# Optimization experiments

Hardware: AMD Instinct MI355X
Metric: run time of the kernel (lower is better)

The kernel has to match this reference:

```python
import jax, jax.numpy as jnp
import numpy as np

# gen_dx_bx([-30,30,0.15], [-15,15,0.15])
DX = jnp.array([0.15, 0.15], dtype=jnp.float32)
BX = jnp.array([-29.925, -14.925], dtype=jnp.float32)


def _pairwise_dist(a, b):
    # torch.cdist p=2: [Na,2] x [Nb,2] -> [Na,Nb]
    return jnp.sqrt(jnp.sum((a[:, None, :] - b[None, :, :]) ** 2, axis=-1))


def _single(match, position, semantic, pts, ins, typ):
    # match [M,M] (M=N+1 with dustbin), position [N,2], semantic [C,N],
    # pts [G,2], ins [G] int, typ [G] int. Assumes mask is all-ones (set in setup_inputs).
    N = position.shape[0]
    M = match.shape[0]
    G = pts.shape[0]
    C = semantic.shape[0]

    pos = position * DX + BX                      # grid -> meters
    cd = _pairwise_dist(pos, pts)                 # [N,G]
    nearest = cd.argmin(-1).astype(jnp.int32)     # [N]
    cdist_mean = jnp.mean(cd.min(-1))             # mean of per-pred nearest-GT distance
    dist_map = _pairwise_dist(pos, pos)           # [N,N]
    nmax = nearest.max()

    # precompute, for every gt index g, whether any pred maps to it and the
    # closest such pred (torch: idx_pred_next[cdist[idx_pred_next, g].argmin()])
    assign = nearest[:, None] == jnp.arange(G, dtype=jnp.int32)[None, :]  # [N,G]
    exists_g = assign.any(0)                                              # [G]
    best_pred_g = jnp.where(assign, cd, jnp.inf).argmin(0).astype(jnp.int32)  # [G]

    def walk(start_gt):
        # greedy forward walk along gt indices; replicates the python while-loop,
        # including torch's negative-index wrap (idx % G) for idx_gt_next = -1.
        def cond(st):
            return ~st[2]

        def body(st):
            idx, steps, done, res = st
            is_end = idx >= nmax
            g_next_raw = jnp.where(is_end, jnp.int32(-1), idx + 1)
            g_next = jnp.mod(g_next_raw, G)
            ex = (~is_end) & exists_g[g_next]  # nearest==-1 never holds in torch
            same = ins[jnp.mod(idx, G)] == ins[g_next]
            matched = ex & same
            stop = matched | (~same) | (steps >= G + 2)  # safety bound
            res_new = jnp.where(matched, best_pred_g[g_next], jnp.int32(-1))
            return (g_next_raw, steps + jnp.int32(1), stop, res_new)

        st = (start_gt, jnp.int32(0), jnp.bool_(False), jnp.int32(-1))
        return jax.lax.while_loop(cond, body, st)[3]

    next_pred = jax.vmap(walk)(nearest)  # [N], -1 means no match (dustbin later)

    # build match_gt [M,M]
    A = jnp.zeros((M, M), dtype=match.dtype)
    valid = next_pred >= 0
    cols = jnp.where(valid, next_pred, 0)
    A = A.at[jnp.arange(N), cols].max(valid.astype(match.dtype))

    # resolve columns matched by multiple rows: keep the row closest in dist_map
    Acols = A[:, :N]
    col_sum = Acols.sum(0)
    dist_pad = jnp.concatenate([dist_map, jnp.full((1, N), jnp.inf, dist_map.dtype)], 0)  # [M,N]
    keep = jnp.where(Acols > 0, dist_pad, jnp.inf).argmin(0)  # [N]
    onehot = (jnp.arange(M)[:, None] == keep[None, :]).astype(match.dtype)
    Acols = jnp.where(col_sum[None, :] > 1, onehot, Acols)
    A = A.at[:, :N].set(Acols)

    # unmatched pred rows -> dustbin column; unmatched pred cols -> dustbin row
    row_sum = A[:N].sum(1)
    A = A.at[:N, M - 1].set(jnp.where(row_sum == 0, 1.0, A[:N, M - 1]))
    col_sum2 = A[:, :N].sum(0)
    A = A.at[M - 1, :N].set(jnp.where(col_sum2 == 0, 1.0, A[M - 1, :N]))

    # semantic gt: one-hot of the type of each pred's nearest gt point
    cls = typ[nearest]  # [N]
    semantic_gt = (jnp.arange(C)[:, None] == cls[None, :]).astype(semantic.dtype)  # [C,N]

    # NLL match loss (torch transposes then feeds NLLLoss: loss = -match[j, target[j]])
    tgt_b = A.argmax(0)  # per-column gt row
    tgt_f = A.argmax(1)  # per-row gt col
    j = jnp.arange(M - 1)
    loss_b = -jnp.mean(match[j, tgt_b[: M - 1]])
    loss_f = -jnp.mean(match[j, tgt_f[: M - 1]])
    match_loss = 0.5 * (loss_f + loss_b)

    sem_loss = -jnp.mean(semantic[semantic_gt.argmax(0), jnp.arange(N)])
    return cdist_mean, match_loss, sem_loss, A, semantic_gt


def setup_inputs() -> dict:
    key = jax.random.key(0)
    ks = jax.random.split(key, 5)
    B, N, G, C, NI = 4, 2048, 1024, 3, 32
    # log-probability score matrix with dustbin (Sinkhorn-style output)
    matches = jax.nn.log_softmax(jax.random.normal(ks[0], (B, N + 1, N + 1), jnp.float32), axis=-1)
    # predicted vertex grid coords on the 400x200 BEV grid
    positions = jax.random.uniform(ks[1], (B, N, 2), jnp.float32) * jnp.array([400.0, 200.0], jnp.float32)
    semantics = jax.nn.log_softmax(jax.random.normal(ks[2], (B, C, N), jnp.float32), axis=1)
    masks = jnp.ones((B, N, 1), jnp.float32)
    # gt points in meters within the BEV range
    gt_pts = (jax.random.uniform(ks[3], (B, G, 2), jnp.float32) - 0.5) * jnp.array([60.0, 30.0], jnp.float32)
    # sorted instance ids -> contiguous runs like the original per-instance list build
    gt_ins = jnp.sort(jax.random.randint(ks[4], (B, G), 0, NI), axis=-1).astype(jnp.int32)
    gt_type = (gt_ins % C).astype(jnp.int32)
    return {"matches": matches, "positions": positions, "semantics": semantics,
            "masks": masks, "gt_pts": gt_pts, "gt_ins": gt_ins, "gt_type": gt_type}


def reference(matches, positions, semantics, masks, gt_pts, gt_ins, gt_type):
    cm, ml, sl, mg, sg = jax.vmap(_single)(matches, positions, semantics, gt_pts, gt_ins, gt_type)
    # reduction='mean'
    return jnp.mean(cm), jnp.mean(ml), jnp.mean(sl), mg, sg
```

## Files before the change

### kernel.cpp

```cpp
#include <hip/hip_runtime.h>
#include <math.h>

#define BB 4
#define NN 2048
#define GG 1024
#define CC 3
#define MM 2049

typedef unsigned long long u64;
#define KEY_EMPTY 0xFFFFFFFFFFFFFFFFULL

struct Ws {
  int   nearest[BB * NN];
  u64   best_key[BB * GG];
  u64   keep_key[BB * NN];
  int   next_pred[BB * NN];
  int   col_cnt[BB * NN];
  int   nmax[BB];
  float cdist_sum[BB];
  float sem_sum[BB];
  float lossf_sum[BB];
  float lossb_sum[BB];
};

__device__ __forceinline__ float posx(float p) { return __fadd_rn(__fmul_rn(p, 0.15f), -29.925f); }
__device__ __forceinline__ float posy(float p) { return __fadd_rn(__fmul_rn(p, 0.15f), -14.925f); }
__device__ __forceinline__ float pdist(float ax, float ay, float bx, float by) {
  float dx = __fsub_rn(ax, bx);
  float dy = __fsub_rn(ay, by);
  return __fsqrt_rn(__fadd_rn(__fmul_rn(dx, dx), __fmul_rn(dy, dy)));
}
__device__ __forceinline__ u64 pack_key(float d, int i) {
  return ((u64)__float_as_uint(d) << 32) | (unsigned int)i;
}


__global__ void k_zero(float* __restrict__ out, int n) {
  int n4 = n >> 2;
  float4 z = make_float4(0.f, 0.f, 0.f, 0.f);
  for (int t = blockIdx.x * blockDim.x + threadIdx.x; t < n4; t += gridDim.x * blockDim.x)
    reinterpret_cast<float4*>(out)[t] = z;
  int t = blockIdx.x * blockDim.x + threadIdx.x;
  int tail = n & 3;
  if (t < tail) out[n4 * 4 + t] = 0.f;
}

__global__ void k_init(Ws* ws) {
  int t = blockIdx.x * blockDim.x + threadIdx.x;
  if (t < BB * NN) {
    ws->col_cnt[t] = 0;
    ws->keep_key[t] = KEY_EMPTY;
  }
  if (t < BB * GG) ws->best_key[t] = KEY_EMPTY;
  if (t < BB) {
    ws->nmax[t] = 0;
    ws->cdist_sum[t] = 0.f;
    ws->sem_sum[t] = 0.f;
    ws->lossf_sum[t] = 0.f;
    ws->lossb_sum[t] = 0.f;
  }
}

__global__ __launch_bounds__(256) void k_nearest(const float* __restrict__ positions,
                                                 const float* __restrict__ gt_pts,
                                                 const int* __restrict__ gt_type,
                                                 const float* __restrict__ semantics,
                                                 Ws* ws, float* __restrict__ out) {
  __shared__ float spts[GG * 2];
  __shared__ float sred[4];
  __shared__ int   sredi[4];
  const int bpb = NN / 256;
  int b = blockIdx.x / bpb;
  int i = (blockIdx.x % bpb) * 256 + threadIdx.x;

  for (int t = threadIdx.x; t < GG * 2; t += 256) spts[t] = gt_pts[b * GG * 2 + t];
  __syncthreads();

  float px = posx(positions[(size_t)(b * NN + i) * 2 + 0]);
  float py = posy(positions[(size_t)(b * NN + i) * 2 + 1]);

  float dmin = INFINITY;
  int gmin = 0;
  #pragma unroll 4
  for (int g = 0; g < GG; ++g) {
    float d = pdist(px, py, spts[2 * g], spts[2 * g + 1]);
    if (d < dmin) { dmin = d; gmin = g; }
  }
  ws->nearest[b * NN + i] = gmin;
  atomicMin(&ws->best_key[b * GG + gmin], pack_key(dmin, i));

  int cls = gt_type[b * GG + gmin];
  float* sg = out + 3 + (size_t)BB * MM * MM;
  sg[(size_t)b * CC * NN + 0 * NN + i] = (cls == 0) ? 1.f : 0.f;
  sg[(size_t)b * CC * NN + 1 * NN + i] = (cls == 1) ? 1.f : 0.f;
  sg[(size_t)b * CC * NN + 2 * NN + i] = (cls == 2) ? 1.f : 0.f;
  float sem = semantics[(size_t)b * CC * NN + (size_t)cls * NN + i];

  int lane = threadIdx.x & 63, w = threadIdx.x >> 6;

  float v = dmin;
  #pragma unroll
  for (int o = 32; o > 0; o >>= 1) v += __shfl_down(v, o, 64);
  if (lane == 0) sred[w] = v;
  __syncthreads();
  if (threadIdx.x == 0) atomicAdd(&ws->cdist_sum[b], sred[0] + sred[1] + sred[2] + sred[3]);
  __syncthreads();

  v = sem;
  #pragma unroll
  for (int o = 32; o > 0; o >>= 1) v += __shfl_down(v, o, 64);
  if (lane == 0) sred[w] = v;
  __syncthreads();
  if (threadIdx.x == 0) atomicAdd(&ws->sem_sum[b], sred[0] + sred[1] + sred[2] + sred[3]);
  __syncthreads();

  int m = gmin;
  #pragma unroll
  for (int o = 32; o > 0; o >>= 1) m = max(m, __shfl_down(m, o, 64));
  if (lane == 0) sredi[w] = m;
  __syncthreads();
  if (threadIdx.x == 0)
    atomicMax(&ws->nmax[b], max(max(sredi[0], sredi[1]), max(sredi[2], sredi[3])));
}

__global__ __launch_bounds__(256) void k_walk(const int* __restrict__ gt_ins,
                                              const float* __restrict__ positions, Ws* ws) {
  __shared__ int sins[GG];
  __shared__ int sbest[GG];
  const int bpb = NN / 256;
  int b = blockIdx.x / bpb;
  int i = (blockIdx.x % bpb) * 256 + threadIdx.x;

  for (int t = threadIdx.x; t < GG; t += 256) {
    sins[t] = gt_ins[b * GG + t];
    u64 k = ws->best_key[b * GG + t];
    sbest[t] = (k == KEY_EMPTY) ? -1 : (int)(k & 0xFFFFFFFFULL);
  }
  __syncthreads();

  int nmax = ws->nmax[b];
  int idx = ws->nearest[b * NN + i];
  int steps = 0, res = -1;
  while (true) {
    bool is_end = idx >= nmax;
    int gnr = is_end ? -1 : idx + 1;
    int gn = gnr & (GG - 1);
    bool ex = (!is_end) && (sbest[gn] >= 0);
    bool same = sins[idx & (GG - 1)] == sins[gn];
    bool matched = ex && same;
    res = matched ? sbest[gn] : -1;
    bool stop = matched || (!same) || (steps >= GG + 2);
    idx = gnr;
    ++steps;
    if (stop) break;
  }
  ws->next_pred[b * NN + i] = res;
  if (res >= 0) {
    atomicAdd(&ws->col_cnt[b * NN + res], 1);
    const float* pb = positions + (size_t)b * NN * 2;
    float d = pdist(posx(pb[2 * i]), posy(pb[2 * i + 1]),
                    posx(pb[2 * res]), posy(pb[2 * res + 1]));
    atomicMin(&ws->keep_key[b * NN + res], pack_key(d, i));
  }
}

__global__ __launch_bounds__(256) void k_scatter(Ws* ws, float* __restrict__ out) {
  const int bpb = NN / 256;
  int b = blockIdx.x / bpb;
  int i = (blockIdx.x % bpb) * 256 + threadIdx.x;

  float* A = out + 3 + (size_t)b * MM * MM;

  int j = ws->next_pred[b * NN + i];
  bool surv = (j >= 0) && ((int)(ws->keep_key[b * NN + j] & 0xFFFFFFFFULL) == i);
  if (surv) A[(size_t)i * MM + j] = 1.0f;
  else      A[(size_t)i * MM + (MM - 1)] = 1.0f;

  if (ws->col_cnt[b * NN + i] == 0)
    A[(size_t)(MM - 1) * MM + i] = 1.0f;
}

__global__ __launch_bounds__(256) void k_loss(const float* __restrict__ matches, Ws* ws) {
  __shared__ float sred[4];
  const int bpb = NN / 256;
  int b = blockIdx.x / bpb;
  int k = (blockIdx.x % bpb) * 256 + threadIdx.x;

  int j = ws->next_pred[b * NN + k];
  bool surv = (j >= 0) && ((int)(ws->keep_key[b * NN + j] & 0xFFFFFFFFULL) == k);
  int tf = surv ? j : (MM - 1);
  float vf = matches[(size_t)b * MM * MM + (size_t)k * MM + tf];

  int cnt = ws->col_cnt[b * NN + k];
  int tb = (cnt > 0) ? (int)(ws->keep_key[b * NN + k] & 0xFFFFFFFFULL) : (MM - 1);
  float vb = matches[(size_t)b * MM * MM + (size_t)k * MM + tb];

  int lane = threadIdx.x & 63, w = threadIdx.x >> 6;

  float v = vf;
  #pragma unroll
  for (int o = 32; o > 0; o >>= 1) v += __shfl_down(v, o, 64);
  if (lane == 0) sred[w] = v;
  __syncthreads();
  if (threadIdx.x == 0) atomicAdd(&ws->lossf_sum[b], sred[0] + sred[1] + sred[2] + sred[3]);
  __syncthreads();

  v = vb;
  #pragma unroll
  for (int o = 32; o > 0; o >>= 1) v += __shfl_down(v, o, 64);
  if (lane == 0) sred[w] = v;
  __syncthreads();
  if (threadIdx.x == 0) atomicAdd(&ws->lossb_sum[b], sred[0] + sred[1] + sred[2] + sred[3]);
}

__global__ void k_final(Ws* ws, float* __restrict__ out) {
  if (threadIdx.x == 0 && blockIdx.x == 0) {
    float cm = 0.f, ml = 0.f, sl = 0.f;
    for (int b = 0; b < BB; ++b) {
      cm += ws->cdist_sum[b] / (float)NN;
      float lf = -(ws->lossf_sum[b] / (float)(MM - 1));
      float lb = -(ws->lossb_sum[b] / (float)(MM - 1));
      ml += 0.5f * (lf + lb);
      sl += -(ws->sem_sum[b] / (float)NN);
    }
    out[0] = cm / (float)BB;
    out[1] = ml / (float)BB;
    out[2] = sl / (float)BB;
  }
}

extern "C" void kernel_launch(void* const* d_in, const int* in_sizes, int n_in,
                              void* d_out, int out_size, void* d_ws, size_t ws_size,
                              hipStream_t stream) {
  (void)in_sizes; (void)n_in; (void)ws_size;
  const float* matches   = (const float*)d_in[0];
  const float* positions = (const float*)d_in[1];
  const float* semantics = (const float*)d_in[2];
  const float* gt_pts    = (const float*)d_in[4];
  const int*   gt_ins    = (const int*)d_in[5];
  const int*   gt_type   = (const int*)d_in[6];
  float* out = (float*)d_out;
  Ws* ws = (Ws*)d_ws;

  k_zero<<<2048, 256, 0, stream>>>(out, out_size);
  k_init<<<(BB * NN + 255) / 256, 256, 0, stream>>>(ws);
  k_nearest<<<BB * (NN / 256), 256, 0, stream>>>(positions, gt_pts, gt_type, semantics, ws, out);
  k_walk<<<BB * (NN / 256), 256, 0, stream>>>(gt_ins, positions, ws);
  k_scatter<<<BB * (NN / 256), 256, 0, stream>>>(ws, out);
  k_loss<<<BB * (NN / 256), 256, 0, stream>>>(matches, ws);
  k_final<<<1, 64, 0, stream>>>(ws, out);
}
```

Before: 171.6 us.

## Split nearest-GT search across blocks, fuse scatter/loss, use memset and smaller blocks

The nearest-GT search is split into 8 chunks of GT points per pred. Each chunk is handled by its own block and combined through a packed atomicMin key, so the launch goes from 32 blocks to 256. The per-pred bookkeeping moves to a separate 64-thread kernel. The scatter and loss kernels are merged, the custom zero kernel is replaced with hipMemsetAsync, and the walk and post kernels use 64-thread blocks to spread across more CUs. The split adds an extra kernel launch and more atomics, and ties are still broken by the lowest index because the key packs distance with the index.

```diff
diff --git a/kernel.cpp b/kernel.cpp
--- a/kernel.cpp
+++ b/kernel.cpp
@@ -6,14 +6,17 @@
 #define GG 1024
 #define CC 3
 #define MM 2049
+#define SP 8
+#define CH (GG / SP)
 
 typedef unsigned long long u64;
 #define KEY_EMPTY 0xFFFFFFFFFFFFFFFFULL
 
 struct Ws {
-  int   nearest[BB * NN];
+  u64   near_key[BB * NN];
   u64   best_key[BB * GG];
   u64   keep_key[BB * NN];
+  int   nearest[BB * NN];
   int   next_pred[BB * NN];
   int   col_cnt[BB * NN];
   int   nmax[BB];
@@ -35,21 +38,12 @@
 }
 
 
-__global__ void k_zero(float* __restrict__ out, int n) {
-  int n4 = n >> 2;
-  float4 z = make_float4(0.f, 0.f, 0.f, 0.f);
-  for (int t = blockIdx.x * blockDim.x + threadIdx.x; t < n4; t += gridDim.x * blockDim.x)
-    reinterpret_cast<float4*>(out)[t] = z;
-  int t = blockIdx.x * blockDim.x + threadIdx.x;
-  int tail = n & 3;
-  if (t < tail) out[n4 * 4 + t] = 0.f;
-}
-
 __global__ void k_init(Ws* ws) {
   int t = blockIdx.x * blockDim.x + threadIdx.x;
   if (t < BB * NN) {
+    ws->near_key[t] = KEY_EMPTY;
+    ws->keep_key[t] = KEY_EMPTY;
     ws->col_cnt[t] = 0;
-    ws->keep_key[t] = KEY_EMPTY;
   }
   if (t < BB * GG) ws->best_key[t] = KEY_EMPTY;
   if (t < BB) {
@@ -61,19 +55,16 @@
   }
 }
 
-__global__ __launch_bounds__(256) void k_nearest(const float* __restrict__ positions,
-                                                 const float* __restrict__ gt_pts,
-                                                 const int* __restrict__ gt_type,
-                                                 const float* __restrict__ semantics,
-                                                 Ws* ws, float* __restrict__ out) {
-  __shared__ float spts[GG * 2];
-  __shared__ float sred[4];
-  __shared__ int   sredi[4];
-  const int bpb = NN / 256;
-  int b = blockIdx.x / bpb;
-  int i = (blockIdx.x % bpb) * 256 + threadIdx.x;
-
-  for (int t = threadIdx.x; t < GG * 2; t += 256) spts[t] = gt_pts[b * GG * 2 + t];
+__global__ __launch_bounds__(256) void k_near1(const float* __restrict__ positions,
+                                               const float* __restrict__ gt_pts, Ws* ws) {
+  __shared__ float spts[CH * 2];
+  const int cpb = NN / 256;
+  int b = blockIdx.x / (cpb * SP);
+  int r = blockIdx.x % (cpb * SP);
+  int i = (r / SP) * 256 + threadIdx.x;
+  int g0 = (r % SP) * CH;
+
+  spts[threadIdx.x] = gt_pts[b * GG * 2 + g0 * 2 + threadIdx.x];
   __syncthreads();
 
   float px = posx(positions[(size_t)(b * NN + i) * 2 + 0]);
@@ -82,59 +73,65 @@
   float dmin = INFINITY;
   int gmin = 0;
   #pragma unroll 4
-  for (int g = 0; g < GG; ++g) {
+  for (int g = 0; g < CH; ++g) {
     float d = pdist(px, py, spts[2 * g], spts[2 * g + 1]);
     if (d < dmin) { dmin = d; gmin = g; }
   }
-  ws->nearest[b * NN + i] = gmin;
-  atomicMin(&ws->best_key[b * GG + gmin], pack_key(dmin, i));
-
-  int cls = gt_type[b * GG + gmin];
+  atomicMin(&ws->near_key[b * NN + i], pack_key(dmin, g0 + gmin));
+}
+
+__global__ __launch_bounds__(64) void k_near2(const int* __restrict__ gt_type,
+                                              const float* __restrict__ semantics,
+                                              Ws* ws, float* __restrict__ out) {
+  int b = blockIdx.x >> 5;
+  int i = (blockIdx.x & 31) * 64 + threadIdx.x;
+
+  u64 key = ws->near_key[b * NN + i];
+  float dmin = __uint_as_float((unsigned int)(key >> 32));
+  int g = (int)(key & 0xFFFFFFFFULL);
+
+  ws->nearest[b * NN + i] = g;
+  atomicMin(&ws->best_key[b * GG + g], pack_key(dmin, i));
+
+  int cls = gt_type[b * GG + g];
   float* sg = out + 3 + (size_t)BB * MM * MM;
   sg[(size_t)b * CC * NN + 0 * NN + i] = (cls == 0) ? 1.f : 0.f;
   sg[(size_t)b * CC * NN + 1 * NN + i] = (cls == 1) ? 1.f : 0.f;
   sg[(size_t)b * CC * NN + 2 * NN + i] = (cls == 2) ? 1.f : 0.f;
   float sem = semantics[(size_t)b * CC * NN + (size_t)cls * NN + i];
 
-  int lane = threadIdx.x & 63, w = threadIdx.x >> 6;
-
   float v = dmin;
   #pragma unroll
   for (int o = 32; o > 0; o >>= 1) v += __shfl_down(v, o, 64);
-  if (lane == 0) sred[w] = v;
-  __syncthreads();
-  if (threadIdx.x == 0) atomicAdd(&ws->cdist_sum[b], sred[0] + sred[1] + sred[2] + sred[3]);
-  __syncthreads();
+  if (threadIdx.x == 0) atomicAdd(&ws->cdist_sum[b], v);
 
   v = sem;
   #pragma unroll
   for (int o = 32; o > 0; o >>= 1) v += __shfl_down(v, o, 64);
-  if (lane == 0) sred[w] = v;
-  __syncthreads();
-  if (threadIdx.x == 0) atomicAdd(&ws->sem_sum[b], sred[0] + sred[1] + sred[2] + sred[3]);
-  __syncthreads();
-
-  int m = gmin;
+  if (threadIdx.x == 0) atomicAdd(&ws->sem_sum[b], v);
+
+  int m = g;
   #pragma unroll
   for (int o = 32; o > 0; o >>= 1) m = max(m, __shfl_down(m, o, 64));
-  if (lane == 0) sredi[w] = m;
-  __syncthreads();
-  if (threadIdx.x == 0)
-    atomicMax(&ws->nmax[b], max(max(sredi[0], sredi[1]), max(sredi[2], sredi[3])));
-}
-
-__global__ __launch_bounds__(256) void k_walk(const int* __restrict__ gt_ins,
-                                              const float* __restrict__ positions, Ws* ws) {
+  if (threadIdx.x == 0) atomicMax(&ws->nmax[b], m);
+}
+
+__global__ __launch_bounds__(64) void k_walk(const int* __restrict__ gt_ins,
+                                             const float* __restrict__ positions, Ws* ws) {
   __shared__ int sins[GG];
   __shared__ int sbest[GG];
-  const int bpb = NN / 256;
-  int b = blockIdx.x / bpb;
-  int i = (blockIdx.x % bpb) * 256 + threadIdx.x;
-
-  for (int t = threadIdx.x; t < GG; t += 256) {
-    sins[t] = gt_ins[b * GG + t];
-    u64 k = ws->best_key[b * GG + t];
-    sbest[t] = (k == KEY_EMPTY) ? -1 : (int)(k & 0xFFFFFFFFULL);
+  int b = blockIdx.x >> 5;
+  int i = (blockIdx.x & 31) * 64 + threadIdx.x;
+
+  {
+    const int4* src = reinterpret_cast<const int4*>(gt_ins + b * GG);
+    int4* dst = reinterpret_cast<int4*>(sins);
+    for (int t = threadIdx.x; t < GG / 4; t += 64) dst[t] = src[t];
+    const u64* bk = ws->best_key + b * GG;
+    for (int t = threadIdx.x; t < GG; t += 64) {
+      u64 k = bk[t];
+      sbest[t] = (k == KEY_EMPTY) ? -1 : (int)(k & 0xFFFFFFFFULL);
+    }
   }
   __syncthreads();
 
@@ -164,10 +161,10 @@
   }
 }
 
-__global__ __launch_bounds__(256) void k_scatter(Ws* ws, float* __restrict__ out) {
-  const int bpb = NN / 256;
-  int b = blockIdx.x / bpb;
-  int i = (blockIdx.x % bpb) * 256 + threadIdx.x;
+__global__ __launch_bounds__(64) void k_post(const float* __restrict__ matches,
+                                             Ws* ws, float* __restrict__ out) {
+  int b = blockIdx.x >> 5;
+  int i = (blockIdx.x & 31) * 64 + threadIdx.x;
 
   float* A = out + 3 + (size_t)b * MM * MM;
 
@@ -176,41 +173,23 @@
   if (surv) A[(size_t)i * MM + j] = 1.0f;
   else      A[(size_t)i * MM + (MM - 1)] = 1.0f;
 
-  if (ws->col_cnt[b * NN + i] == 0)
-    A[(size_t)(MM - 1) * MM + i] = 1.0f;
-}
-
-__global__ __launch_bounds__(256) void k_loss(const float* __restrict__ matches, Ws* ws) {
-  __shared__ float sred[4];
-  const int bpb = NN / 256;
-  int b = blockIdx.x / bpb;
-  int k = (blockIdx.x % bpb) * 256 + threadIdx.x;
-
-  int j = ws->next_pred[b * NN + k];
-  bool surv = (j >= 0) && ((int)(ws->keep_key[b * NN + j] & 0xFFFFFFFFULL) == k);
+  int cnt = ws->col_cnt[b * NN + i];
+  if (cnt == 0) A[(size_t)(MM - 1) * MM + i] = 1.0f;
+
   int tf = surv ? j : (MM - 1);
-  float vf = matches[(size_t)b * MM * MM + (size_t)k * MM + tf];
-
-  int cnt = ws->col_cnt[b * NN + k];
-  int tb = (cnt > 0) ? (int)(ws->keep_key[b * NN + k] & 0xFFFFFFFFULL) : (MM - 1);
-  float vb = matches[(size_t)b * MM * MM + (size_t)k * MM + tb];
-
-  int lane = threadIdx.x & 63, w = threadIdx.x >> 6;
+  float vf = matches[(size_t)b * MM * MM + (size_t)i * MM + tf];
+  int tb = (cnt > 0) ? (int)(ws->keep_key[b * NN + i] & 0xFFFFFFFFULL) : (MM - 1);
+  float vb = matches[(size_t)b * MM * MM + (size_t)i * MM + tb];
 
   float v = vf;
   #pragma unroll
   for (int o = 32; o > 0; o >>= 1) v += __shfl_down(v, o, 64);
-  if (lane == 0) sred[w] = v;
-  __syncthreads();
-  if (threadIdx.x == 0) atomicAdd(&ws->lossf_sum[b], sred[0] + sred[1] + sred[2] + sred[3]);
-  __syncthreads();
+  if (threadIdx.x == 0) atomicAdd(&ws->lossf_sum[b], v);
 
   v = vb;
   #pragma unroll
   for (int o = 32; o > 0; o >>= 1) v += __shfl_down(v, o, 64);
-  if (lane == 0) sred[w] = v;
-  __syncthreads();
-  if (threadIdx.x == 0) atomicAdd(&ws->lossb_sum[b], sred[0] + sred[1] + sred[2] + sred[3]);
+  if (threadIdx.x == 0) atomicAdd(&ws->lossb_sum[b], v);
 }
 
 __global__ void k_final(Ws* ws, float* __restrict__ out) {
@@ -242,11 +221,11 @@
   float* out = (float*)d_out;
   Ws* ws = (Ws*)d_ws;
 
-  k_zero<<<2048, 256, 0, stream>>>(out, out_size);
+  hipMemsetAsync(d_out, 0, (size_t)out_size * sizeof(float), stream);
   k_init<<<(BB * NN + 255) / 256, 256, 0, stream>>>(ws);
-  k_nearest<<<BB * (NN / 256), 256, 0, stream>>>(positions, gt_pts, gt_type, semantics, ws, out);
-  k_walk<<<BB * (NN / 256), 256, 0, stream>>>(gt_ins, positions, ws);
-  k_scatter<<<BB * (NN / 256), 256, 0, stream>>>(ws, out);
-  k_loss<<<BB * (NN / 256), 256, 0, stream>>>(matches, ws);
+  k_near1<<<BB * (NN / 256) * SP, 256, 0, stream>>>(positions, gt_pts, ws);
+  k_near2<<<BB * (NN / 64), 64, 0, stream>>>(gt_type, semantics, ws, out);
+  k_walk<<<BB * (NN / 64), 64, 0, stream>>>(gt_ins, positions, ws);
+  k_post<<<BB * (NN / 64), 64, 0, stream>>>(matches, ws, out);
   k_final<<<1, 64, 0, stream>>>(ws, out);
 }
```

Measured after the change: 150.8 us. -12.1%, faster.
